# Kernel optimization log

Hardware: AMD Instinct MI355X
Metric: run time of the kernel (lower is better)

Reference implementation:

```python
import jax, jax.numpy as jnp
import numpy as np

N = 50000      # nodes
E = 800000     # edges
F_IN = 64      # n_features
H = 128        # graph_hidden_layers
LAT = 128      # latent_size
DH = 1024      # dense_hidden_layers
G = 256        # num graphs in batch
EPS = 1e-5


def setup_inputs() -> dict:
    key = jax.random.key(0)
    ks = jax.random.split(key, 32)
    def rn(k, shape, scale=0.05):
        return jax.random.normal(k, shape, dtype=jnp.float32) * scale
    inp = {
        "x": jax.random.normal(ks[0], (N, F_IN), dtype=jnp.float32),
        "origin": jax.random.normal(ks[1], (G, 3), dtype=jnp.float32),
        "direction": jax.random.normal(ks[2], (G, 3), dtype=jnp.float32),
        "edge_index": jax.random.randint(ks[3], (2, E), 0, N, dtype=jnp.int32),
        "batch": jnp.sort(jax.random.randint(ks[4], (N,), 0, G, dtype=jnp.int32)),
        # GCNConv weights
        "W1": rn(ks[5], (F_IN, H)), "b1": jnp.zeros((H,), jnp.float32),
        "W2": rn(ks[6], (H, H)),    "b2": jnp.zeros((H,), jnp.float32),
        "W3": rn(ks[7], (H, LAT)), "b3": jnp.zeros((LAT,), jnp.float32),
        # BatchNorm affine params
        "g1": jnp.ones((H,), jnp.float32),   "be1": jnp.zeros((H,), jnp.float32),
        "g2": jnp.ones((H,), jnp.float32),   "be2": jnp.zeros((H,), jnp.float32),
        "g3": jnp.ones((LAT,), jnp.float32), "be3": jnp.zeros((LAT,), jnp.float32),
        # Dense head: (LAT+6)->DH, then n_dense_layers=2 of DH->DH, then DH->3
        "Wd0": rn(ks[8], (LAT + 6, DH)), "bd0": jnp.zeros((DH,), jnp.float32),
        "Wd1": rn(ks[9], (DH, DH)),      "bd1": jnp.zeros((DH,), jnp.float32),
        "Wd2": rn(ks[10], (DH, DH)),     "bd2": jnp.zeros((DH,), jnp.float32),
        "Wout": rn(ks[11], (DH, 3)),     "bout": jnp.zeros((3,), jnp.float32),
    }
    return inp


def _gcn_conv(x, W, b, src, dst, deg_inv_sqrt):
    """PyG GCNConv with self-loops: D^{-1/2} (A+I) D^{-1/2} x W + b."""
    xW = x @ W  # [N, out]
    norm = deg_inv_sqrt[src] * deg_inv_sqrt[dst]  # [E]
    msg = xW[src] * norm[:, None]                 # gather + scale
    agg = jax.ops.segment_sum(msg, dst, num_segments=N)
    agg = agg + xW * (deg_inv_sqrt * deg_inv_sqrt)[:, None]  # self-loop term
    return agg + b


def _batchnorm(x, gamma, beta):
    m = jnp.mean(x, axis=0)
    v = jnp.mean(jnp.square(x - m), axis=0)
    return (x - m) * jax.lax.rsqrt(v + EPS) * gamma + beta


def reference(x, origin, direction, edge_index, batch,
              W1, b1, W2, b2, W3, b3,
              g1, be1, g2, be2, g3, be3,
              Wd0, bd0, Wd1, bd1, Wd2, bd2, Wout, bout):
    src, dst = edge_index[0], edge_index[1]
    # degree with self-loops (in-degree at dst, matching gcn_norm)
    deg = jax.ops.segment_sum(jnp.ones((E,), jnp.float32), dst, num_segments=N) + 1.0
    deg_inv_sqrt = jax.lax.rsqrt(deg)

    h = jax.nn.relu(_batchnorm(_gcn_conv(x, W1, b1, src, dst, deg_inv_sqrt), g1, be1))
    h = jax.nn.relu(_batchnorm(_gcn_conv(h, W2, b2, src, dst, deg_inv_sqrt), g2, be2))
    h = _batchnorm(_gcn_conv(h, W3, b3, src, dst, deg_inv_sqrt), g3, be3)

    # global mean pool over graphs
    sums = jax.ops.segment_sum(h, batch, num_segments=G)
    cnt = jax.ops.segment_sum(jnp.ones((N,), jnp.float32), batch, num_segments=G)
    pooled = sums / jnp.maximum(cnt, 1.0)[:, None]  # [G, LAT]

    z = jnp.concatenate([pooled, origin, direction], axis=1)  # [G, LAT+6]
    z = jax.nn.relu(z @ Wd0 + bd0)
    z = jax.nn.relu(z @ Wd1 + bd1)
    z = jax.nn.relu(z @ Wd2 + bd2)
    return z @ Wout + bout  # [G, 3]
```

## Files before the change

kernel.cpp:

```cpp
#include <hip/hip_runtime.h>

#define HC 128
#define FIN 64
#define DHID 1024
#define ZK 134
#define ZKP 160

typedef __attribute__((ext_vector_type(8))) short short8;
typedef __attribute__((ext_vector_type(8))) __bf16 bf16x8;
typedef __attribute__((ext_vector_type(4))) float f32x4;
typedef __attribute__((ext_vector_type(8))) unsigned short u16x8;
typedef __attribute__((ext_vector_type(4))) unsigned short u16x4;

union FragU { short8 s; bf16x8 b; u16x8 u; };

__device__ inline unsigned short rne_bf16(float x) {
    union { float f; unsigned u; } v; v.f = x;
    unsigned u = v.u;
    unsigned r = (u + 0x7fffu + ((u >> 16) & 1u)) >> 16;
    return (unsigned short)r;
}
__device__ inline float bf16_to_f(unsigned short h) {
    union { unsigned u; float f; } v; v.u = ((unsigned)h) << 16;
    return v.f;
}

__global__ void k_zero_i(int* p, int n) {
    int i = blockIdx.x * blockDim.x + threadIdx.x;
    if (i < n) p[i] = 0;
}

__global__ void k_deg_i(const int* __restrict__ dst, int* __restrict__ cnt, int E) {
    int i = blockIdx.x * blockDim.x + threadIdx.x;
    if (i < E) atomicAdd(&cnt[dst[i]], 1);
}

__global__ void k_xtobf(const float* __restrict__ x, unsigned short* __restrict__ xb, int n4) {
    int i = blockIdx.x * blockDim.x + threadIdx.x;
    if (i >= n4) return;
    float4 v = ((const float4*)x)[i];
    u16x4 o;
    o[0] = rne_bf16(v.x); o[1] = rne_bf16(v.y);
    o[2] = rne_bf16(v.z); o[3] = rne_bf16(v.w);
    ((u16x4*)xb)[i] = o;
}

__global__ void k_scan1(const int* __restrict__ cnt, int* __restrict__ part,
                        int* __restrict__ bsum, float* __restrict__ dinv, int N) {
    __shared__ int sh[256];
    int t = threadIdx.x, i = blockIdx.x * 256 + t;
    int v = (i < N) ? cnt[i] : 0;
    if (i < N) dinv[i] = rsqrtf((float)v + 1.0f);
    sh[t] = v; __syncthreads();
    #pragma unroll
    for (int off = 1; off < 256; off <<= 1) {
        int tv = (t >= off) ? sh[t - off] : 0;
        __syncthreads();
        sh[t] += tv;
        __syncthreads();
    }
    if (i < N) part[i] = sh[t] - v;
    if (t == 255) bsum[blockIdx.x] = sh[255];
}

__global__ void k_scan2(int* __restrict__ bsum, int nb) {
    __shared__ int sh[256];
    int t = threadIdx.x;
    int v = (t < nb) ? bsum[t] : 0;
    sh[t] = v; __syncthreads();
    #pragma unroll
    for (int off = 1; off < 256; off <<= 1) {
        int tv = (t >= off) ? sh[t - off] : 0;
        __syncthreads();
        sh[t] += tv;
        __syncthreads();
    }
    if (t < nb) bsum[t] = sh[t] - v;
}

__global__ void k_scan3(const int* __restrict__ part, const int* __restrict__ bsum,
                        int* __restrict__ row_start, int* __restrict__ cur, int N) {
    int i = blockIdx.x * 256 + threadIdx.x;
    if (i < N) { row_start[i] = part[i] + bsum[blockIdx.x]; cur[i] = 0; }
}

__global__ void k_scatter(const int* __restrict__ src, const int* __restrict__ dst,
                          const float* __restrict__ dinv, const int* __restrict__ row_start,
                          int* __restrict__ cur, int2* __restrict__ csr, int E) {
    int e = blockIdx.x * blockDim.x + threadIdx.x;
    if (e >= E) return;
    int s = src[e], d = dst[e];
    int pos = row_start[d] + atomicAdd(&cur[d], 1);
    int2 pk; pk.x = s; pk.y = __float_as_int(dinv[s] * dinv[d]);
    csr[pos] = pk;
}

template <int RF> struct BVec;
template <> struct BVec<64>  { using T = u16x4; static const int VPL = 4; };
template <> struct BVec<128> { using T = u16x8; static const int VPL = 8; };

template <int RF>
__global__ __launch_bounds__(256) void k_gather2b(const unsigned short* __restrict__ T,
                                                  const int2* __restrict__ csr,
                                                  const int* __restrict__ row_start,
                                                  const int* __restrict__ cnt,
                                                  const float* __restrict__ dinv,
                                                  unsigned short* __restrict__ agg, int N) {
    using vec = typename BVec<RF>::T;
    constexpr int VPL = BVec<RF>::VPL;
    int tid = threadIdx.x;
    int node = blockIdx.x * 16 + (tid >> 4);
    int q = tid & 15;
    if (node >= N) return;
    int beg = row_start[node];
    int end = beg + cnt[node];
    float d = dinv[node];
    vec sv = ((const vec*)(T + (size_t)node * RF))[q];
    float acc[VPL];
    #pragma unroll
    for (int i = 0; i < VPL; ++i) acc[i] = bf16_to_f(sv[i]) * d * d;
    int j = beg;
    for (; j + 4 <= end; j += 4) {
        int2 e0 = csr[j], e1 = csr[j + 1], e2 = csr[j + 2], e3 = csr[j + 3];
        vec v0 = ((const vec*)(T + (size_t)e0.x * RF))[q];
        vec v1 = ((const vec*)(T + (size_t)e1.x * RF))[q];
        vec v2 = ((const vec*)(T + (size_t)e2.x * RF))[q];
        vec v3 = ((const vec*)(T + (size_t)e3.x * RF))[q];
        float n0 = __int_as_float(e0.y), n1 = __int_as_float(e1.y);
        float n2 = __int_as_float(e2.y), n3 = __int_as_float(e3.y);
        #pragma unroll
        for (int i = 0; i < VPL; ++i) {
            acc[i] += bf16_to_f(v0[i]) * n0 + bf16_to_f(v1[i]) * n1
                    + bf16_to_f(v2[i]) * n2 + bf16_to_f(v3[i]) * n3;
        }
    }
    for (; j < end; ++j) {
        int2 e0 = csr[j];
        vec v0 = ((const vec*)(T + (size_t)e0.x * RF))[q];
        float n0 = __int_as_float(e0.y);
        #pragma unroll
        for (int i = 0; i < VPL; ++i) acc[i] += bf16_to_f(v0[i]) * n0;
    }
    vec o;
    #pragma unroll
    for (int i = 0; i < VPL; ++i) o[i] = rne_bf16(acc[i]);
    ((vec*)(agg + (size_t)node * RF))[q] = o;
}

__global__ void k_bn_reduce(const unsigned short* __restrict__ x, float* __restrict__ stat, int N) {
    int f = threadIdx.x & (HC - 1);
    int half = threadIdx.x >> 7;
    int rpb = (N + gridDim.x - 1) / gridDim.x;
    int r0 = blockIdx.x * rpb;
    int r1 = min(N, r0 + rpb);
    float s = 0.f, ss = 0.f;
    for (int r = r0 + half; r < r1; r += 2) {
        float v = bf16_to_f(x[(size_t)r * HC + f]);
        s += v; ss += v * v;
    }
    __shared__ float sh[256], shq[256];
    sh[threadIdx.x] = s; shq[threadIdx.x] = ss;
    __syncthreads();
    if (half == 0) {
        atomicAdd(&stat[f],      sh[threadIdx.x] + sh[threadIdx.x + HC]);
        atomicAdd(&stat[HC + f], shq[threadIdx.x] + shq[threadIdx.x + HC]);
    }
}

__global__ void k_pool(const unsigned short* __restrict__ h, const int* __restrict__ batch,
                       const float* __restrict__ stat, const float* __restrict__ gam,
                       const float* __restrict__ bet, float invN,
                       float* __restrict__ pooled, float* __restrict__ cnt, int N) {
    int t = threadIdx.x;
    float m = stat[t] * invN;
    float var = stat[HC + t] * invN - m * m;
    float istd = rsqrtf(var + 1e-5f);
    float scv = gam[t] * istd;
    float shv = bet[t] - m * scv;
    int rpb = (N + gridDim.x - 1) / gridDim.x;
    int r0 = blockIdx.x * rpb;
    int r1 = min(N, r0 + rpb);
    if (r0 >= r1) return;
    int curb = batch[r0];
    float acc = 0.f; float c = 0.f;
    for (int r = r0; r < r1; ++r) {
        int b = batch[r];
        if (b != curb) {
            atomicAdd(&pooled[curb * HC + t], acc);
            if (t == 0) atomicAdd(&cnt[curb], c);
            curb = b; acc = 0.f; c = 0.f;
        }
        acc += bf16_to_f(h[(size_t)r * HC + t]) * scv + shv;
        c += 1.f;
    }
    atomicAdd(&pooled[curb * HC + t], acc);
    if (t == 0) atomicAdd(&cnt[curb], c);
}

__global__ void k_build_z(const float* __restrict__ pooled, const float* __restrict__ cnt,
                          const float* __restrict__ origin, const float* __restrict__ dir,
                          float* __restrict__ z, int G) {
    int g = blockIdx.x;
    int t = threadIdx.x;
    if (t >= ZKP) return;
    float v = 0.f;
    if (t < HC) {
        float c = fmaxf(cnt[g], 1.0f);
        v = pooled[g * HC + t] / c;
    } else if (t < HC + 3) {
        v = origin[g * 3 + (t - HC)];
    } else if (t < HC + 6) {
        v = dir[g * 3 + (t - HC - 3)];
    }
    z[g * ZKP + t] = v;
}

__global__ void k_wprep_all(const float* __restrict__ W1, const float* __restrict__ W2,
                            const float* __restrict__ W3,
                            unsigned short* __restrict__ w1h, unsigned short* __restrict__ w1l,
                            unsigned short* __restrict__ w2h, unsigned short* __restrict__ w2l,
                            unsigned short* __restrict__ w3h, unsigned short* __restrict__ w3l) {
    int i = blockIdx.x * blockDim.x + threadIdx.x;
    const float* W; unsigned short *th, *tl; int K, idx;
    if (i < FIN * HC)           { W = W1; th = w1h; tl = w1l; K = FIN; idx = i; }
    else if (i < FIN*HC + HC*HC){ W = W2; th = w2h; tl = w2l; K = HC;  idx = i - FIN*HC; }
    else if (i < FIN*HC + 2*HC*HC){ W = W3; th = w3h; tl = w3l; K = HC; idx = i - FIN*HC - HC*HC; }
    else return;
    int k = idx >> 7, n = idx & (HC - 1);
    float w = W[idx];
    unsigned short h = rne_bf16(w);
    th[n * K + k] = h;
    tl[n * K + k] = rne_bf16(w - bf16_to_f(h));
}

__global__ __launch_bounds__(256) void k_wprep2(const float* __restrict__ W,
                                                unsigned short* __restrict__ th,
                                                unsigned short* __restrict__ tl,
                                                int K, int KP, int NC) {
    __shared__ float tile[32][33];
    int kt = blockIdx.x * 32, nt = blockIdx.y * 32;
    int tx = threadIdx.x & 31, ty0 = threadIdx.x >> 5;
    #pragma unroll
    for (int i = 0; i < 4; ++i) {
        int ty = ty0 + i * 8;
        int k = kt + ty;
        float v = (k < K) ? W[(size_t)k * NC + nt + tx] : 0.f;
        tile[ty][tx] = v;
    }
    __syncthreads();
    #pragma unroll
    for (int i = 0; i < 4; ++i) {
        int ty = ty0 + i * 8;
        int n = nt + ty;
        int k = kt + tx;
        float w = tile[tx][ty];
        unsigned short h = rne_bf16(w);
        th[(size_t)n * KP + k] = h;
        tl[(size_t)n * KP + k] = rne_bf16(w - bf16_to_f(h));
    }
}

template <int KK, bool BN>
__global__ __launch_bounds__(256) void gemm_node(const unsigned short* __restrict__ A,
                                                 const unsigned short* __restrict__ wth,
                                                 const unsigned short* __restrict__ wtl,
                                                 const float* __restrict__ stat,
                                                 const float* __restrict__ gam,
                                                 const float* __restrict__ bet,
                                                 float invN,
                                                 unsigned short* __restrict__ C, int M) {
    constexpr int KS = KK / 32;
    int tid = threadIdx.x;
    int lane = tid & 63, wid = tid >> 6;
    int rw = wid & 1, cw = wid >> 1;
    int l15 = lane & 15, l4 = lane >> 4;
    int m0 = blockIdx.x * 32 + rw * 16;
    int cbase = cw * 64;

    FragU bh[4][KS], bl[4][KS];
    #pragma unroll
    for (int ct = 0; ct < 4; ++ct) {
        int n = cbase + ct * 16 + l15;
        #pragma unroll
        for (int ks = 0; ks < KS; ++ks) {
            int k = ks * 32 + l4 * 8;
            bh[ct][ks].s = *(const short8*)(wth + (size_t)n * KK + k);
            bl[ct][ks].s = *(const short8*)(wtl + (size_t)n * KK + k);
        }
    }
    if (m0 >= M) return;

    int arow = m0 + l15;
    f32x4 zero = {0.f, 0.f, 0.f, 0.f};
    f32x4 acc[4] = {zero, zero, zero, zero};

    #pragma unroll
    for (int ks = 0; ks < KS; ++ks) {
        int k0 = ks * 32 + l4 * 8;
        u16x8 a = *(const u16x8*)(A + (size_t)arow * KK + k0);
        float av[8];
        #pragma unroll
        for (int i = 0; i < 8; ++i) av[i] = bf16_to_f(a[i]);
        if (BN) {
            #pragma unroll
            for (int i = 0; i < 8; ++i) {
                int k = k0 + i;
                float m = stat[k] * invN;
                float var = stat[HC + k] * invN - m * m;
                float istd = rsqrtf(var + 1e-5f);
                float sc = gam[k] * istd;
                av[i] = fmaxf(av[i] * sc + (bet[k] - m * sc), 0.f);
            }
        }
        FragU ah, al;
        #pragma unroll
        for (int i = 0; i < 8; ++i) {
            unsigned short h = rne_bf16(av[i]);
            ah.s[i] = (short)h;
            al.s[i] = (short)rne_bf16(av[i] - bf16_to_f(h));
        }
        #pragma unroll
        for (int ct = 0; ct < 4; ++ct) {
            acc[ct] = __builtin_amdgcn_mfma_f32_16x16x32_bf16(ah.b, bh[ct][ks].b, acc[ct], 0, 0, 0);
            acc[ct] = __builtin_amdgcn_mfma_f32_16x16x32_bf16(ah.b, bl[ct][ks].b, acc[ct], 0, 0, 0);
            acc[ct] = __builtin_amdgcn_mfma_f32_16x16x32_bf16(al.b, bh[ct][ks].b, acc[ct], 0, 0, 0);
        }
    }

    #pragma unroll
    for (int ct = 0; ct < 4; ++ct) {
        int col = cbase + ct * 16 + l15;
        #pragma unroll
        for (int r = 0; r < 4; ++r) {
            int row = m0 + l4 * 4 + r;
            C[(size_t)row * HC + col] = rne_bf16(acc[ct][r]);
        }
    }
}

__global__ __launch_bounds__(256) void gemm_head_sk(const float* __restrict__ A,
                                                    const unsigned short* __restrict__ wth,
                                                    const unsigned short* __restrict__ wtl,
                                                    float* __restrict__ Cpart,
                                                    int M, int N, int K, int slice) {
    int tid = threadIdx.x;
    int lane = tid & 63, wid = tid >> 6;
    int rw = wid & 1, cw = wid >> 1;
    int l15 = lane & 15, l4 = lane >> 4;
    int m0 = blockIdx.y * 32 + rw * 16;
    int cb = blockIdx.x * 64 + cw * 32;
    int z = blockIdx.z;
    int kbeg = z * slice;
    int kend = min(K, kbeg + slice);
    if (m0 >= M) return;

    int arow = m0 + l15;
    f32x4 zero = {0.f, 0.f, 0.f, 0.f};
    f32x4 acc[2] = {zero, zero};

    for (int k0 = kbeg; k0 < kend; k0 += 32) {
        int ka = k0 + l4 * 8;
        const float4 p0 = *(const float4*)(A + (size_t)arow * K + ka);
        const float4 p1 = *(const float4*)(A + (size_t)arow * K + ka + 4);
        float av[8] = {p0.x, p0.y, p0.z, p0.w, p1.x, p1.y, p1.z, p1.w};
        FragU ah, al;
        #pragma unroll
        for (int i = 0; i < 8; ++i) {
            unsigned short h = rne_bf16(av[i]);
            ah.s[i] = (short)h;
            al.s[i] = (short)rne_bf16(av[i] - bf16_to_f(h));
        }
        #pragma unroll
        for (int ct = 0; ct < 2; ++ct) {
            int n = cb + ct * 16 + l15;
            FragU bh, bl;
            bh.s = *(const short8*)(wth + (size_t)n * K + ka);
            bl.s = *(const short8*)(wtl + (size_t)n * K + ka);
            acc[ct] = __builtin_amdgcn_mfma_f32_16x16x32_bf16(ah.b, bh.b, acc[ct], 0, 0, 0);
            acc[ct] = __builtin_amdgcn_mfma_f32_16x16x32_bf16(ah.b, bl.b, acc[ct], 0, 0, 0);
            acc[ct] = __builtin_amdgcn_mfma_f32_16x16x32_bf16(al.b, bh.b, acc[ct], 0, 0, 0);
        }
    }

    float* Cz = Cpart + (size_t)z * M * N;
    #pragma unroll
    for (int ct = 0; ct < 2; ++ct) {
        int col = cb + ct * 16 + l15;
        #pragma unroll
        for (int r = 0; r < 4; ++r) {
            int row = m0 + l4 * 4 + r;
            Cz[(size_t)row * N + col] = acc[ct][r];
        }
    }
}

__global__ void k_reduce_br(const float* __restrict__ part, const float* __restrict__ bias,
                            float* __restrict__ C, int MN, int Nmask, int NZ) {
    int i = (blockIdx.x * blockDim.x + threadIdx.x) * 4;
    if (i >= MN) return;
    float4 acc = *(const float4*)(part + i);
    for (int zz = 1; zz < NZ; ++zz) {
        float4 p = *(const float4*)(part + (size_t)zz * MN + i);
        acc.x += p.x; acc.y += p.y; acc.z += p.z; acc.w += p.w;
    }
    int n = i & Nmask;
    acc.x += bias[n]; acc.y += bias[n + 1]; acc.z += bias[n + 2]; acc.w += bias[n + 3];
    acc.x = fmaxf(acc.x, 0.f); acc.y = fmaxf(acc.y, 0.f);
    acc.z = fmaxf(acc.z, 0.f); acc.w = fmaxf(acc.w, 0.f);
    *(float4*)(C + i) = acc;
}

__global__ void k_dense_out(const float* __restrict__ z, const float* __restrict__ W,
                            const float* __restrict__ b, float* __restrict__ out, int K) {
    int g = blockIdx.x;
    const float* zr = z + (size_t)g * K;
    float a0 = 0.f, a1 = 0.f, a2 = 0.f;
    for (int k = threadIdx.x; k < K; k += blockDim.x) {
        float zv = zr[k];
        a0 += zv * W[k * 3 + 0];
        a1 += zv * W[k * 3 + 1];
        a2 += zv * W[k * 3 + 2];
    }
    __shared__ float s[768];
    s[threadIdx.x] = a0; s[256 + threadIdx.x] = a1; s[512 + threadIdx.x] = a2;
    __syncthreads();
    for (int off = 128; off > 0; off >>= 1) {
        if ((int)threadIdx.x < off) {
            s[threadIdx.x]       += s[threadIdx.x + off];
            s[256 + threadIdx.x] += s[256 + threadIdx.x + off];
            s[512 + threadIdx.x] += s[512 + threadIdx.x + off];
        }
        __syncthreads();
    }
    if (threadIdx.x == 0) {
        out[g * 3 + 0] = s[0]   + b[0];
        out[g * 3 + 1] = s[256] + b[1];
        out[g * 3 + 2] = s[512] + b[2];
    }
}

extern "C" void kernel_launch(void* const* d_in, const int* in_sizes, int n_in,
                              void* d_out, int out_size, void* d_ws, size_t ws_size,
                              hipStream_t stream) {
    const float* x         = (const float*)d_in[0];
    const float* origin    = (const float*)d_in[1];
    const float* direction = (const float*)d_in[2];
    const int*   eidx      = (const int*)d_in[3];
    const int*   batch     = (const int*)d_in[4];
    const float* W1 = (const float*)d_in[5];
    const float* W2 = (const float*)d_in[7];
    const float* W3 = (const float*)d_in[9];
    const float* g1 = (const float*)d_in[11]; const float* be1 = (const float*)d_in[12];
    const float* g2 = (const float*)d_in[13]; const float* be2 = (const float*)d_in[14];
    const float* g3 = (const float*)d_in[15]; const float* be3 = (const float*)d_in[16];
    const float* Wd0 = (const float*)d_in[17]; const float* bd0 = (const float*)d_in[18];
    const float* Wd1 = (const float*)d_in[19]; const float* bd1 = (const float*)d_in[20];
    const float* Wd2 = (const float*)d_in[21]; const float* bd2 = (const float*)d_in[22];
    const float* Wout = (const float*)d_in[23]; const float* bout = (const float*)d_in[24];
    float* out = (float*)d_out;

    const int N = in_sizes[4];
    const int E = in_sizes[3] / 2;
    const int G = in_sizes[1] / 3;
    const int* src = eidx;
    const int* dst = eidx + E;

    char* ws = (char*)d_ws;
    size_t off = 0;
    auto alloc = [&](size_t nbytes) -> void* {
        void* p = (void*)(ws + off);
        off += (nbytes + 255) & ~(size_t)255;
        return p;
    };
    float* colstats = (float*)alloc(3 * 2 * HC * 4);
    float* pooled   = (float*)alloc((size_t)G * HC * 4);
    float* cntf     = (float*)alloc((size_t)G * 4);
    const size_t zeroBytes = 3 * 2 * HC * 4 + (size_t)G * HC * 4 + (size_t)G * 4;

    float* dinv     = (float*)alloc((size_t)N * 4);
    int*   degcnt   = (int*)alloc((size_t)N * 4);
    int*   part     = (int*)alloc((size_t)N * 4);
    int*   bsum     = (int*)alloc(256 * 4);
    int*   row_start= (int*)alloc((size_t)N * 4);
    int*   cur      = (int*)alloc((size_t)N * 4);
    int2*  csr      = (int2*)alloc((size_t)E * 8);
    unsigned short* xb   = (unsigned short*)alloc((size_t)N * FIN * 2);
    unsigned short* aggx = (unsigned short*)alloc((size_t)N * FIN * 2);
    unsigned short* tabA = (unsigned short*)alloc((size_t)N * HC * 2);
    unsigned short* tabB = (unsigned short*)alloc((size_t)N * HC * 2);
    unsigned short* wt1h = (unsigned short*)alloc((size_t)FIN * HC * 2);
    unsigned short* wt1l = (unsigned short*)alloc((size_t)FIN * HC * 2);
    unsigned short* wt2h = (unsigned short*)alloc((size_t)HC * HC * 2);
    unsigned short* wt2l = (unsigned short*)alloc((size_t)HC * HC * 2);
    unsigned short* wt3h = (unsigned short*)alloc((size_t)HC * HC * 2);
    unsigned short* wt3l = (unsigned short*)alloc((size_t)HC * HC * 2);
    unsigned short* wd0h = (unsigned short*)alloc((size_t)DHID * ZKP * 2);
    unsigned short* wd0l = (unsigned short*)alloc((size_t)DHID * ZKP * 2);
    unsigned short* wd1h = (unsigned short*)alloc((size_t)DHID * DHID * 2);
    unsigned short* wd1l = (unsigned short*)alloc((size_t)DHID * DHID * 2);
    unsigned short* wd2h = (unsigned short*)alloc((size_t)DHID * DHID * 2);
    unsigned short* wd2l = (unsigned short*)alloc((size_t)DHID * DHID * 2);
    float* zbuf     = (float*)alloc((size_t)G * ZKP * 4);
    float* t0       = (float*)alloc((size_t)G * DHID * 4);
    float* t1       = (float*)alloc((size_t)G * DHID * 4);
    float* kpart    = (float*)alloc((size_t)8 * G * DHID * 4);
    (void)ws_size;

    const int nScanBlk = (N + 255) / 256;
    const int gemmBlk = (N + 31) / 32;
    const int gatherBlk = (N + 15) / 16;
    const float invN = 1.0f / (float)N;

    hipMemsetAsync(colstats, 0, zeroBytes, stream);

    k_xtobf<<<(N * FIN / 4 + 255) / 256, 256, 0, stream>>>(x, xb, N * FIN / 4);
    k_wprep_all<<<(FIN * HC + 2 * HC * HC + 255) / 256, 256, 0, stream>>>(
        W1, W2, W3, wt1h, wt1l, wt2h, wt2l, wt3h, wt3l);
    k_wprep2<<<dim3(ZKP / 32, DHID / 32), 256, 0, stream>>>(Wd0, wd0h, wd0l, ZK, ZKP, DHID);
    k_wprep2<<<dim3(DHID / 32, DHID / 32), 256, 0, stream>>>(Wd1, wd1h, wd1l, DHID, DHID, DHID);
    k_wprep2<<<dim3(DHID / 32, DHID / 32), 256, 0, stream>>>(Wd2, wd2h, wd2l, DHID, DHID, DHID);

    k_zero_i<<<nScanBlk, 256, 0, stream>>>(degcnt, N);
    k_deg_i<<<(E + 255) / 256, 256, 0, stream>>>(dst, degcnt, E);
    k_scan1<<<nScanBlk, 256, 0, stream>>>(degcnt, part, bsum, dinv, N);
    k_scan2<<<1, 256, 0, stream>>>(bsum, nScanBlk);
    k_scan3<<<nScanBlk, 256, 0, stream>>>(part, bsum, row_start, cur, N);
    k_scatter<<<(E + 255) / 256, 256, 0, stream>>>(src, dst, dinv, row_start, cur, csr, E);

    k_gather2b<FIN><<<gatherBlk, 256, 0, stream>>>(xb, csr, row_start, degcnt, dinv, aggx, N);
    gemm_node<FIN, false><<<gemmBlk, 256, 0, stream>>>(aggx, wt1h, wt1l, nullptr, nullptr,
                                                       nullptr, invN, tabA, N);
    k_bn_reduce<<<256, 256, 0, stream>>>(tabA, colstats + 0 * 2 * HC, N);

    gemm_node<HC, true><<<gemmBlk, 256, 0, stream>>>(tabA, wt2h, wt2l, colstats + 0 * 2 * HC,
                                                     g1, be1, invN, tabB, N);
    k_gather2b<HC><<<gatherBlk, 256, 0, stream>>>(tabB, csr, row_start, degcnt, dinv, tabA, N);
    k_bn_reduce<<<256, 256, 0, stream>>>(tabA, colstats + 1 * 2 * HC, N);

    gemm_node<HC, true><<<gemmBlk, 256, 0, stream>>>(tabA, wt3h, wt3l, colstats + 1 * 2 * HC,
                                                     g2, be2, invN, tabB, N);
    k_gather2b<HC><<<gatherBlk, 256, 0, stream>>>(tabB, csr, row_start, degcnt, dinv, tabA, N);
    k_bn_reduce<<<256, 256, 0, stream>>>(tabA, colstats + 2 * 2 * HC, N);

    k_pool<<<512, HC, 0, stream>>>(tabA, batch, colstats + 2 * 2 * HC, g3, be3, invN,
                                   pooled, cntf, N);
    k_build_z<<<G, 192, 0, stream>>>(pooled, cntf, origin, direction, zbuf, G);

    const int MN = G * DHID;
    const int rblk = (MN / 4 + 255) / 256;

    gemm_head_sk<<<dim3(DHID / 64, (G + 31) / 32, 5), 256, 0, stream>>>(
        zbuf, wd0h, wd0l, kpart, G, DHID, ZKP, 32);
    k_reduce_br<<<rblk, 256, 0, stream>>>(kpart, bd0, t0, MN, DHID - 1, 5);

    gemm_head_sk<<<dim3(DHID / 64, (G + 31) / 32, 8), 256, 0, stream>>>(
        t0, wd1h, wd1l, kpart, G, DHID, DHID, 128);
    k_reduce_br<<<rblk, 256, 0, stream>>>(kpart, bd1, t1, MN, DHID - 1, 8);

    gemm_head_sk<<<dim3(DHID / 64, (G + 31) / 32, 8), 256, 0, stream>>>(
        t1, wd2h, wd2l, kpart, G, DHID, DHID, 128);
    k_reduce_br<<<rblk, 256, 0, stream>>>(kpart, bd2, t0, MN, DHID - 1, 8);

    k_dense_out<<<G, 256, 0, stream>>>(t0, Wout, bout, out, DHID);
}
```

Before: 456.6 us.

## Unroll gather by 8, split BN apply out of node GEMM, drop A-low MFMA

Widens the CSR gather loop to eight outstanding neighbor loads per iteration for more memory-level parallelism. Moves the BatchNorm+ReLU out of the node GEMM into separate stats and apply kernels, so the GEMM no longer recomputes per-element statistics. The new GEMM uses 512 threads, covers 64 rows per block and keeps fewer weight fragments per wave. It also drops the A-low correction MFMA because the activations are already bf16. This adds two extra kernel launches and a full read-write pass over the activation table per layer.

```diff
diff --git a/kernel.cpp b/kernel.cpp
--- a/kernel.cpp
+++ b/kernel.cpp
@@ -120,21 +120,30 @@
     #pragma unroll
     for (int i = 0; i < VPL; ++i) acc[i] = bf16_to_f(sv[i]) * d * d;
     int j = beg;
-    for (; j + 4 <= end; j += 4) {
-        int2 e0 = csr[j], e1 = csr[j + 1], e2 = csr[j + 2], e3 = csr[j + 3];
+    for (; j + 8 <= end; j += 8) {
+        int2 e[8];
+        #pragma unroll
+        for (int u = 0; u < 8; ++u) e[u] = csr[j + u];
+        vec v[8];
+        #pragma unroll
+        for (int u = 0; u < 8; ++u) v[u] = ((const vec*)(T + (size_t)e[u].x * RF))[q];
+        #pragma unroll
+        for (int u = 0; u < 8; ++u) {
+            float nn = __int_as_float(e[u].y);
+            #pragma unroll
+            for (int i = 0; i < VPL; ++i) acc[i] += bf16_to_f(v[u][i]) * nn;
+        }
+    }
+    for (; j + 2 <= end; j += 2) {
+        int2 e0 = csr[j], e1 = csr[j + 1];
         vec v0 = ((const vec*)(T + (size_t)e0.x * RF))[q];
         vec v1 = ((const vec*)(T + (size_t)e1.x * RF))[q];
-        vec v2 = ((const vec*)(T + (size_t)e2.x * RF))[q];
-        vec v3 = ((const vec*)(T + (size_t)e3.x * RF))[q];
         float n0 = __int_as_float(e0.y), n1 = __int_as_float(e1.y);
-        float n2 = __int_as_float(e2.y), n3 = __int_as_float(e3.y);
-        #pragma unroll
-        for (int i = 0; i < VPL; ++i) {
-            acc[i] += bf16_to_f(v0[i]) * n0 + bf16_to_f(v1[i]) * n1
-                    + bf16_to_f(v2[i]) * n2 + bf16_to_f(v3[i]) * n3;
-        }
-    }
-    for (; j < end; ++j) {
+        #pragma unroll
+        for (int i = 0; i < VPL; ++i)
+            acc[i] += bf16_to_f(v0[i]) * n0 + bf16_to_f(v1[i]) * n1;
+    }
+    if (j < end) {
         int2 e0 = csr[j];
         vec v0 = ((const vec*)(T + (size_t)e0.x * RF))[q];
         float n0 = __int_as_float(e0.y);
@@ -165,6 +174,33 @@
         atomicAdd(&stat[f],      sh[threadIdx.x] + sh[threadIdx.x + HC]);
         atomicAdd(&stat[HC + f], shq[threadIdx.x] + shq[threadIdx.x + HC]);
     }
+}
+
+__global__ void k_bn_stats2(const float* __restrict__ stat, const float* __restrict__ gam,
+                            const float* __restrict__ bet, float invN,
+                            float* __restrict__ scale, float* __restrict__ shift) {
+    int f = threadIdx.x;
+    float m = stat[f] * invN;
+    float var = stat[HC + f] * invN - m * m;
+    float istd = rsqrtf(var + 1e-5f);
+    float sc = gam[f] * istd;
+    scale[f] = sc;
+    shift[f] = bet[f] - m * sc;
+}
+
+__global__ void k_bn_apply2(unsigned short* __restrict__ t, const float* __restrict__ scale,
+                            const float* __restrict__ shift, int total8) {
+    int i = blockIdx.x * blockDim.x + threadIdx.x;
+    if (i >= total8) return;
+    int k0 = (i * 8) & (HC - 1);
+    u16x8 v = ((const u16x8*)t)[i];
+    u16x8 o;
+    #pragma unroll
+    for (int j = 0; j < 8; ++j) {
+        float f = bf16_to_f(v[j]) * scale[k0 + j] + shift[k0 + j];
+        o[j] = rne_bf16(fmaxf(f, 0.f));
+    }
+    ((u16x8*)t)[i] = o;
 }
 
 __global__ void k_pool(const unsigned short* __restrict__ h, const int* __restrict__ batch,
@@ -260,26 +296,21 @@
     }
 }
 
-template <int KK, bool BN>
-__global__ __launch_bounds__(256) void gemm_node(const unsigned short* __restrict__ A,
-                                                 const unsigned short* __restrict__ wth,
-                                                 const unsigned short* __restrict__ wtl,
-                                                 const float* __restrict__ stat,
-                                                 const float* __restrict__ gam,
-                                                 const float* __restrict__ bet,
-                                                 float invN,
-                                                 unsigned short* __restrict__ C, int M) {
+template <int KK>
+__global__ __launch_bounds__(512) void gemm_node2(const unsigned short* __restrict__ A,
+                                                  const unsigned short* __restrict__ wth,
+                                                  const unsigned short* __restrict__ wtl,
+                                                  unsigned short* __restrict__ C, int M) {
     constexpr int KS = KK / 32;
     int tid = threadIdx.x;
     int lane = tid & 63, wid = tid >> 6;
-    int rw = wid & 1, cw = wid >> 1;
+    int rw = wid & 1, cg = wid >> 1;
     int l15 = lane & 15, l4 = lane >> 4;
-    int m0 = blockIdx.x * 32 + rw * 16;
-    int cbase = cw * 64;
-
-    FragU bh[4][KS], bl[4][KS];
-    #pragma unroll
-    for (int ct = 0; ct < 4; ++ct) {
+    int cbase = cg * 32;
+
+    FragU bh[2][KS], bl[2][KS];
+    #pragma unroll
+    for (int ct = 0; ct < 2; ++ct) {
         int n = cbase + ct * 16 + l15;
         #pragma unroll
         for (int ks = 0; ks < KS; ++ks) {
@@ -288,52 +319,35 @@
             bl[ct][ks].s = *(const short8*)(wtl + (size_t)n * KK + k);
         }
     }
-    if (m0 >= M) return;
-
-    int arow = m0 + l15;
-    f32x4 zero = {0.f, 0.f, 0.f, 0.f};
-    f32x4 acc[4] = {zero, zero, zero, zero};
-
-    #pragma unroll
-    for (int ks = 0; ks < KS; ++ks) {
-        int k0 = ks * 32 + l4 * 8;
-        u16x8 a = *(const u16x8*)(A + (size_t)arow * KK + k0);
-        float av[8];
-        #pragma unroll
-        for (int i = 0; i < 8; ++i) av[i] = bf16_to_f(a[i]);
-        if (BN) {
+
+    #pragma unroll
+    for (int rt = 0; rt < 2; ++rt) {
+        int m0 = blockIdx.x * 64 + rt * 32 + rw * 16;
+        if (m0 < M) {
+            int arow = min(m0 + l15, M - 1);
+            f32x4 zero = {0.f, 0.f, 0.f, 0.f};
+            f32x4 acc[2] = {zero, zero};
             #pragma unroll
-            for (int i = 0; i < 8; ++i) {
-                int k = k0 + i;
-                float m = stat[k] * invN;
-                float var = stat[HC + k] * invN - m * m;
-                float istd = rsqrtf(var + 1e-5f);
-                float sc = gam[k] * istd;
-                av[i] = fmaxf(av[i] * sc + (bet[k] - m * sc), 0.f);
+            for (int ks = 0; ks < KS; ++ks) {
+                int k0 = ks * 32 + l4 * 8;
+                FragU a;
+                a.u = *(const u16x8*)(A + (size_t)arow * KK + k0);
+                #pragma unroll
+                for (int ct = 0; ct < 2; ++ct) {
+                    acc[ct] = __builtin_amdgcn_mfma_f32_16x16x32_bf16(a.b, bh[ct][ks].b, acc[ct], 0, 0, 0);
+                    acc[ct] = __builtin_amdgcn_mfma_f32_16x16x32_bf16(a.b, bl[ct][ks].b, acc[ct], 0, 0, 0);
+                }
             }
-        }
-        FragU ah, al;
-        #pragma unroll
-        for (int i = 0; i < 8; ++i) {
-            unsigned short h = rne_bf16(av[i]);
-            ah.s[i] = (short)h;
-            al.s[i] = (short)rne_bf16(av[i] - bf16_to_f(h));
-        }
-        #pragma unroll
-        for (int ct = 0; ct < 4; ++ct) {
-            acc[ct] = __builtin_amdgcn_mfma_f32_16x16x32_bf16(ah.b, bh[ct][ks].b, acc[ct], 0, 0, 0);
-            acc[ct] = __builtin_amdgcn_mfma_f32_16x16x32_bf16(ah.b, bl[ct][ks].b, acc[ct], 0, 0, 0);
-            acc[ct] = __builtin_amdgcn_mfma_f32_16x16x32_bf16(al.b, bh[ct][ks].b, acc[ct], 0, 0, 0);
-        }
-    }
-
-    #pragma unroll
-    for (int ct = 0; ct < 4; ++ct) {
-        int col = cbase + ct * 16 + l15;
-        #pragma unroll
-        for (int r = 0; r < 4; ++r) {
-            int row = m0 + l4 * 4 + r;
-            C[(size_t)row * HC + col] = rne_bf16(acc[ct][r]);
+            #pragma unroll
+            for (int ct = 0; ct < 2; ++ct) {
+                int col = cbase + ct * 16 + l15;
+                #pragma unroll
+                for (int r = 0; r < 4; ++r) {
+                    int row = m0 + l4 * 4 + r;
+                    if (row < M)
+                        C[(size_t)row * HC + col] = rne_bf16(acc[ct][r]);
+                }
+            }
         }
     }
 }
@@ -500,6 +514,8 @@
     unsigned short* wd1l = (unsigned short*)alloc((size_t)DHID * DHID * 2);
     unsigned short* wd2h = (unsigned short*)alloc((size_t)DHID * DHID * 2);
     unsigned short* wd2l = (unsigned short*)alloc((size_t)DHID * DHID * 2);
+    float* bnscale  = (float*)alloc(HC * 4);
+    float* bnshift  = (float*)alloc(HC * 4);
     float* zbuf     = (float*)alloc((size_t)G * ZKP * 4);
     float* t0       = (float*)alloc((size_t)G * DHID * 4);
     float* t1       = (float*)alloc((size_t)G * DHID * 4);
@@ -507,8 +523,9 @@
     (void)ws_size;
 
     const int nScanBlk = (N + 255) / 256;
-    const int gemmBlk = (N + 31) / 32;
+    const int gemmBlk = (N + 63) / 64;
     const int gatherBlk = (N + 15) / 16;
+    const int total8 = N * HC / 8;
     const float invN = 1.0f / (float)N;
 
     hipMemsetAsync(colstats, 0, zeroBytes, stream);
@@ -528,17 +545,18 @@
     k_scatter<<<(E + 255) / 256, 256, 0, stream>>>(src, dst, dinv, row_start, cur, csr, E);
 
     k_gather2b<FIN><<<gatherBlk, 256, 0, stream>>>(xb, csr, row_start, degcnt, dinv, aggx, N);
-    gemm_node<FIN, false><<<gemmBlk, 256, 0, stream>>>(aggx, wt1h, wt1l, nullptr, nullptr,
-                                                       nullptr, invN, tabA, N);
+    gemm_node2<FIN><<<gemmBlk, 512, 0, stream>>>(aggx, wt1h, wt1l, tabA, N);
     k_bn_reduce<<<256, 256, 0, stream>>>(tabA, colstats + 0 * 2 * HC, N);
 
-    gemm_node<HC, true><<<gemmBlk, 256, 0, stream>>>(tabA, wt2h, wt2l, colstats + 0 * 2 * HC,
-                                                     g1, be1, invN, tabB, N);
+    k_bn_stats2<<<1, HC, 0, stream>>>(colstats + 0 * 2 * HC, g1, be1, invN, bnscale, bnshift);
+    k_bn_apply2<<<(total8 + 255) / 256, 256, 0, stream>>>(tabA, bnscale, bnshift, total8);
+    gemm_node2<HC><<<gemmBlk, 512, 0, stream>>>(tabA, wt2h, wt2l, tabB, N);
     k_gather2b<HC><<<gatherBlk, 256, 0, stream>>>(tabB, csr, row_start, degcnt, dinv, tabA, N);
     k_bn_reduce<<<256, 256, 0, stream>>>(tabA, colstats + 1 * 2 * HC, N);
 
-    gemm_node<HC, true><<<gemmBlk, 256, 0, stream>>>(tabA, wt3h, wt3l, colstats + 1 * 2 * HC,
-                                                     g2, be2, invN, tabB, N);
+    k_bn_stats2<<<1, HC, 0, stream>>>(colstats + 1 * 2 * HC, g2, be2, invN, bnscale, bnshift);
+    k_bn_apply2<<<(total8 + 255) / 256, 256, 0, stream>>>(tabA, bnscale, bnshift, total8);
+    gemm_node2<HC><<<gemmBlk, 512, 0, stream>>>(tabA, wt3h, wt3l, tabB, N);
     k_gather2b<HC><<<gatherBlk, 256, 0, stream>>>(tabB, csr, row_start, degcnt, dinv, tabA, N);
     k_bn_reduce<<<256, 256, 0, stream>>>(tabA, colstats + 2 * 2 * HC, N);
 
```

Measured after the change: 451.7 us. No clear change (-1.1%).
